# Performance work log

Measured on AMD Instinct MI355X. Metric: run time of the kernel, lower is better.

## Reference

```python
import jax, jax.numpy as jnp
import numpy as np


def setup_inputs() -> dict:
    key = jax.random.key(0)
    ks = jax.random.split(key, 20)
    B, T, E, U, D, O = 64, 2048, 256, 256, 256, 32000
    s = lambda k, shp, fan: (jax.random.normal(k, shp, jnp.float32) * (1.0 / np.sqrt(fan)))
    return {
        'inputs': jax.random.normal(ks[0], (B, D), jnp.float32),
        'stm': jax.random.normal(ks[1], (B, U), jnp.float32),
        'x_seq': jax.random.normal(ks[2], (B, T, E), jnp.float32),
        'V_a': s(ks[3], (U + E,), U + E),
        'W_a': s(ks[4], (U + E, U + E), U + E),
        'W_r': s(ks[5], (D, U), D), 'U_r': s(ks[6], (U, U), U), 'C_r': s(ks[7], (E, U), E), 'b_r': jnp.zeros((U,), jnp.float32),
        'W_z': s(ks[8], (D, U), D), 'U_z': s(ks[9], (U, U), U), 'C_z': s(ks[10], (E, U), E), 'b_z': jnp.zeros((U,), jnp.float32),
        'W_p': s(ks[11], (D, U), D), 'U_p': s(ks[12], (U, U), U), 'C_p': s(ks[13], (E, U), E), 'b_p': jnp.zeros((U,), jnp.float32),
        'W_o': s(ks[14], (D, O), D), 'U_o': s(ks[15], (U, O), U), 'C_o': s(ks[16], (E, O), E), 'b_o': jnp.zeros((O,), jnp.float32),
    }


def reference(inputs, stm, x_seq, V_a, W_a,
              W_r, U_r, C_r, b_r,
              W_z, U_z, C_z, b_z,
              W_p, U_p, C_p, b_p,
              W_o, U_o, C_o, b_o):
    B, T, E = x_seq.shape
    U = stm.shape[-1]
    # Bahdanau additive attention: concat repeated state with encoder seq
    _stm = jnp.broadcast_to(stm[:, None, :], (B, T, U))          # [B,T,U]
    cat = jnp.concatenate([_stm, x_seq], axis=-1)                 # [B,T,U+E]
    et = jnp.einsum('btc,c->bt', jnp.tanh(jnp.einsum('btc,cd->btd', cat, W_a)), V_a)
    at = jax.nn.softmax(et, axis=1)                               # exp / sum over T
    context = jnp.einsum('bt,bte->be', at, x_seq)                 # [B,E]
    # GRU-style gates conditioned on input, previous state, and context
    rt = jax.nn.sigmoid(inputs @ W_r + stm @ U_r + context @ C_r + b_r)
    zt = jax.nn.sigmoid(inputs @ W_z + stm @ U_z + context @ C_z + b_z)
    s_tp = jnp.tanh(inputs @ W_p + (rt * stm) @ U_p + context @ C_p + b_p)
    st = (1.0 - zt) * stm + zt * s_tp                             # new state [B,U]
    output = jax.nn.softmax(inputs @ W_o + stm @ U_o + context @ C_o + b_o, axis=-1)  # [B,O]
    return output, st
```

## Files before the change

### kernel.cpp

```cpp
#include <hip/hip_runtime.h>
#include <hip/hip_bf16.h>

#define B_ 64
#define T_ 2048
#define E_ 256
#define U_ 256
#define O_ 32000
#define UE_ 512

typedef __attribute__((ext_vector_type(8))) short bf16x8;
typedef __attribute__((ext_vector_type(4))) float f32x4;

__device__ __forceinline__ unsigned short f2bf(float f){
  __hip_bfloat16 h = __float2bfloat16(f);
  return __builtin_bit_cast(unsigned short, h);
}
__device__ __forceinline__ unsigned pk2bf(float a, float b){
  return (unsigned)f2bf(a) | ((unsigned)f2bf(b) << 16);
}
__device__ __forceinline__ bf16x8 pack8(const float* v0, const float* v1){
  float4 x = *(const float4*)v0;
  float4 y = *(const float4*)v1;
  uint4 pk;
  pk.x = pk2bf(x.x, x.y); pk.y = pk2bf(x.z, x.w);
  pk.z = pk2bf(y.x, y.y); pk.w = pk2bf(y.z, y.w);
  return __builtin_bit_cast(bf16x8, pk);
}
__device__ __forceinline__ float ftanh(float x){
  float e = __expf(2.0f*x);
  return 1.0f - 2.0f/(e + 1.0f);
}
__device__ __forceinline__ float fsig(float x){
  return 1.0f/(1.0f + __expf(-x));
}

__global__ __launch_bounds__(256)
void prep_kernel(const float* __restrict__ Wa, const float* __restrict__ stm,
                 unsigned short* __restrict__ bpack, float* __restrict__ sp){
  if (blockIdx.x < 64){
    int idx = blockIdx.x*256 + threadIdx.x;
    int n = idx & 511;
    int ktg = idx >> 9;
    int erow = ktg * 8;
    unsigned short o[8];
#pragma unroll
    for (int i = 0; i < 8; ++i)
      o[i] = f2bf(Wa[(256 + erow + i)*512 + n]);
    uint4 v;
    v.x = (unsigned)o[0] | ((unsigned)o[1] << 16);
    v.y = (unsigned)o[2] | ((unsigned)o[3] << 16);
    v.z = (unsigned)o[4] | ((unsigned)o[5] << 16);
    v.w = (unsigned)o[6] | ((unsigned)o[7] << 16);
    ((uint4*)bpack)[idx] = v;
  } else {
    int tid = threadIdx.x;
    int w = tid >> 6, l = tid & 63, c = l & 15, g = l >> 4;
    int n0 = (blockIdx.x - 64)*64 + w*16;
    f32x4 zero = {0.f,0.f,0.f,0.f};
    f32x4 acc[4];
#pragma unroll
    for (int mt = 0; mt < 4; ++mt) acc[mt] = zero;
#pragma unroll
    for (int ks = 0; ks < 8; ++ks){
      int kg = ks*32 + 8*g;
      bf16x8 a[4];
#pragma unroll
      for (int mt = 0; mt < 4; ++mt){
        const float* ap = stm + (mt*16 + c)*256 + kg;
        a[mt] = pack8(ap, ap + 4);
      }
      const float* bpt = Wa + (size_t)kg*512 + n0 + c;
      float bv[8];
#pragma unroll
      for (int i = 0; i < 8; ++i) bv[i] = bpt[(size_t)i*512];
      uint4 pk;
      pk.x = pk2bf(bv[0], bv[1]); pk.y = pk2bf(bv[2], bv[3]);
      pk.z = pk2bf(bv[4], bv[5]); pk.w = pk2bf(bv[6], bv[7]);
      bf16x8 bfr = __builtin_bit_cast(bf16x8, pk);
#pragma unroll
      for (int mt = 0; mt < 4; ++mt)
        acc[mt] = __builtin_amdgcn_mfma_f32_16x16x32_bf16(a[mt], bfr, acc[mt], 0, 0, 0);
    }
#pragma unroll
    for (int mt = 0; mt < 4; ++mt)
#pragma unroll
      for (int r = 0; r < 4; ++r){
        int m = mt*16 + 4*g + r;
        sp[m*512 + n0 + c] = acc[mt][r];
      }
  }
}

__global__ __launch_bounds__(512, 4)
void et_flash_kernel(const float* __restrict__ xseq, const unsigned short* __restrict__ bpack,
                     const float* __restrict__ va, const float* __restrict__ sp,
                     float* __restrict__ msbuf, float* __restrict__ uctxp){
  __shared__ __align__(16) uint4 sA4[2048];
  __shared__ float sVa[512];
  __shared__ float sSp[512];
  __shared__ float sEt[8][64];
  __shared__ float sE[64];
  int tid = threadIdx.x;
  int w = tid >> 6, l = tid & 63, c = l & 15, g = l >> 4;
  int m0 = blockIdx.x * 64;
  int b  = m0 >> 11;

  const float4* x4 = (const float4*)xseq + (size_t)m0 * 64;
  uint2* sA2 = (uint2*)sA4;
#pragma unroll
  for (int i = 0; i < 8; ++i){
    int p = i*512 + tid;
    int row = p >> 6, kq = p & 63;
    float4 v = x4[row*64 + kq];
    uint2 u;
    u.x = pk2bf(v.x, v.y);
    u.y = pk2bf(v.z, v.w);
    int s = ((row>>4)*8 + (kq>>3))*64 + ((kq>>1)&3)*16 + (row&15);
    sA2[(s ^ ((s>>4)&7))*2 + (kq&1)] = u;
  }
  sVa[tid] = va[tid];
  sSp[tid] = sp[b*512 + tid];
  __syncthreads();

  f32x4 zero = {0.f, 0.f, 0.f, 0.f};
  f32x4 acc[4][4];
#pragma unroll
  for (int mt = 0; mt < 4; ++mt)
#pragma unroll
    for (int tc = 0; tc < 4; ++tc) acc[mt][tc] = zero;

  const bf16x8* bp = (const bf16x8*)bpack;
#pragma unroll
  for (int ks = 0; ks < 8; ++ks){
    bf16x8 aw[4], bx[4];
    int bbase = (ks*4 + g)*512 + w*64 + c;
#pragma unroll
    for (int mt = 0; mt < 4; ++mt)
      aw[mt] = bp[bbase + mt*16];
#pragma unroll
    for (int tc = 0; tc < 4; ++tc){
      int idx = (tc*8 + ks)*64 + l;
      bx[tc] = *(const bf16x8*)&sA4[idx ^ ((idx>>4)&7)];
    }
#pragma unroll
    for (int mt = 0; mt < 4; ++mt)
#pragma unroll
      for (int tc = 0; tc < 4; ++tc)
        acc[mt][tc] = __builtin_amdgcn_mfma_f32_16x16x32_bf16(aw[mt], bx[tc], acc[mt][tc], 0, 0, 0);
  }

  float p[4] = {0.f, 0.f, 0.f, 0.f};
#pragma unroll
  for (int mt = 0; mt < 4; ++mt){
    int nb = w*64 + mt*16 + 4*g;
    float4 vav = *(const float4*)&sVa[nb];
    float4 spv = *(const float4*)&sSp[nb];
#pragma unroll
    for (int tc = 0; tc < 4; ++tc){
#pragma unroll
      for (int r = 0; r < 4; ++r){
        float vv = acc[mt][tc][r] + ((const float*)&spv)[r];
        p[tc] += ((const float*)&vav)[r] * ftanh(vv);
      }
    }
  }
#pragma unroll
  for (int tc = 0; tc < 4; ++tc){
    p[tc] += __shfl_xor(p[tc], 16, 64);
    p[tc] += __shfl_xor(p[tc], 32, 64);
  }
  if (l < 16){
#pragma unroll
    for (int tc = 0; tc < 4; ++tc)
      sEt[w][tc*16 + c] = p[tc];
  }
  __syncthreads();

  if (tid < 64){
    float e = 0.f;
#pragma unroll
    for (int ww = 0; ww < 8; ++ww) e += sEt[ww][tid];
    float m = e;
#pragma unroll
    for (int off = 1; off < 64; off <<= 1) m = fmaxf(m, __shfl_xor(m, off, 64));
    float ex = __expf(e - m);
    float s = ex;
#pragma unroll
    for (int off = 1; off < 64; off <<= 1) s += __shfl_xor(s, off, 64);
    sE[tid] = ex;
    if (tid == 0){
      msbuf[blockIdx.x*2]     = m;
      msbuf[blockIdx.x*2 + 1] = s;
    }
  }
  __syncthreads();

  {
    int e = tid & 255, th = tid >> 8;
    int ks = e >> 5, gg = (e >> 3) & 3, ii = e & 7;
    const unsigned short* sU = (const unsigned short*)sA4;
    float a0 = 0.f;
#pragma unroll
    for (int tt = 0; tt < 32; ++tt){
      int t = th*32 + tt;
      int mt = t >> 4, cc = t & 15;
      int slt = (mt*8 + ks)*64 + gg*16 + cc;
      unsigned short hv = sU[(size_t)(slt ^ ((slt>>4)&7))*8 + ii];
      float xv = __builtin_bit_cast(float, ((unsigned)hv) << 16);
      a0 += sE[t] * xv;
    }
    uctxp[((size_t)blockIdx.x*2 + th)*256 + e] = a0;
  }
}

__global__ void ctx_x1_kernel(const float* __restrict__ msbuf, const float* __restrict__ uctxp,
                              const float* __restrict__ inputs, const float* __restrict__ stm,
                              unsigned short* __restrict__ X1bf){
  int b = blockIdx.x, e = threadIdx.x;
  float M = -INFINITY;
#pragma unroll 4
  for (int j = 0; j < 32; ++j) M = fmaxf(M, msbuf[(32*b + j)*2]);
  float S = 0.f;
  float acc = 0.f;
#pragma unroll 4
  for (int j = 0; j < 32; ++j){
    float wj = __expf(msbuf[(32*b + j)*2] - M);
    S += msbuf[(32*b + j)*2 + 1] * wj;
    size_t base = ((size_t)(32*b + j)*2)*256 + e;
    acc += (uctxp[base] + uctxp[base + 256]) * wj;
  }
  float ctx = acc / S;
  X1bf[b*768 + e]        = f2bf(inputs[b*256 + e]);
  X1bf[b*768 + 256 + e]  = f2bf(stm[b*256 + e]);
  X1bf[b*768 + 512 + e]  = f2bf(ctx);
}

__global__ __launch_bounds__(256)
void gates1_kernel(const unsigned short* __restrict__ X1bf, const float* __restrict__ stm,
                   const float* __restrict__ Wr, const float* __restrict__ Ur,
                   const float* __restrict__ Cr, const float* __restrict__ brr,
                   const float* __restrict__ Wz, const float* __restrict__ Uz,
                   const float* __restrict__ Cz, const float* __restrict__ bzz,
                   const float* __restrict__ Wp, const float* __restrict__ Cp,
                   const float* __restrict__ bpp,
                   float* __restrict__ rs, float* __restrict__ ztb, float* __restrict__ pic){
  int tid = threadIdx.x;
  int w = tid >> 6, l = tid & 63, c = l & 15, g = l >> 4;
  int n0 = blockIdx.x*64 + w*16;
  int gate = n0 >> 8;
  int col0 = n0 & 255;
  const float* W0; const float* W1; const float* W2; const float* bias;
  if (gate == 0){ W0 = Wr; W1 = Ur; W2 = Cr; bias = brr; }
  else if (gate == 1){ W0 = Wz; W1 = Uz; W2 = Cz; bias = bzz; }
  else { W0 = Wp; W1 = nullptr; W2 = Cp; bias = bpp; }

  f32x4 zero = {0.f,0.f,0.f,0.f};
  f32x4 acc[4];
#pragma unroll
  for (int mt = 0; mt < 4; ++mt) acc[mt] = zero;

#pragma unroll
  for (int ph = 0; ph < 3; ++ph){
    const float* src = (ph == 0) ? W0 : (ph == 1) ? W1 : W2;
    if (src == nullptr) continue;
#pragma unroll
    for (int ks = 0; ks < 8; ++ks){
      int kg = ks*32 + 8*g;
      bf16x8 a[4];
#pragma unroll
      for (int mt = 0; mt < 4; ++mt)
        a[mt] = *(const bf16x8*)&X1bf[(mt*16 + c)*768 + ph*256 + kg];
      const float* bpt = src + (size_t)kg*256 + col0 + c;
      float bv[8];
#pragma unroll
      for (int i = 0; i < 8; ++i) bv[i] = bpt[(size_t)i*256];
      uint4 pk;
      pk.x = pk2bf(bv[0], bv[1]); pk.y = pk2bf(bv[2], bv[3]);
      pk.z = pk2bf(bv[4], bv[5]); pk.w = pk2bf(bv[6], bv[7]);
      bf16x8 bfr = __builtin_bit_cast(bf16x8, pk);
#pragma unroll
      for (int mt = 0; mt < 4; ++mt)
        acc[mt] = __builtin_amdgcn_mfma_f32_16x16x32_bf16(a[mt], bfr, acc[mt], 0, 0, 0);
    }
  }

  int n = col0 + c;
  float bi = bias[n];
#pragma unroll
  for (int mt = 0; mt < 4; ++mt)
#pragma unroll
    for (int r = 0; r < 4; ++r){
      int m = mt*16 + 4*g + r;
      float pre = acc[mt][r] + bi;
      if (gate == 0)      rs[m*256 + n]  = fsig(pre) * stm[m*256 + n];
      else if (gate == 1) ztb[m*256 + n] = fsig(pre);
      else                pic[m*256 + n] = pre;
    }
}

__global__ __launch_bounds__(256)
void gates2_kernel(const float* __restrict__ rs, const float* __restrict__ Up,
                   const float* __restrict__ pic, const float* __restrict__ ztb,
                   const float* __restrict__ stm, float* __restrict__ stout){
  int tid = threadIdx.x;
  int w = tid >> 6, l = tid & 63, c = l & 15, g = l >> 4;
  int n0 = blockIdx.x*64 + w*16;
  f32x4 zero = {0.f,0.f,0.f,0.f};
  f32x4 acc[4];
#pragma unroll
  for (int mt = 0; mt < 4; ++mt) acc[mt] = zero;
#pragma unroll
  for (int ks = 0; ks < 8; ++ks){
    int kg = ks*32 + 8*g;
    bf16x8 a[4];
#pragma unroll
    for (int mt = 0; mt < 4; ++mt){
      const float* ap = rs + (mt*16 + c)*256 + kg;
      a[mt] = pack8(ap, ap + 4);
    }
    const float* bpt = Up + (size_t)kg*256 + n0 + c;
    float bv[8];
#pragma unroll
    for (int i = 0; i < 8; ++i) bv[i] = bpt[(size_t)i*256];
    uint4 pk;
    pk.x = pk2bf(bv[0], bv[1]); pk.y = pk2bf(bv[2], bv[3]);
    pk.z = pk2bf(bv[4], bv[5]); pk.w = pk2bf(bv[6], bv[7]);
    bf16x8 bfr = __builtin_bit_cast(bf16x8, pk);
#pragma unroll
    for (int mt = 0; mt < 4; ++mt)
      acc[mt] = __builtin_amdgcn_mfma_f32_16x16x32_bf16(a[mt], bfr, acc[mt], 0, 0, 0);
  }
#pragma unroll
  for (int mt = 0; mt < 4; ++mt)
#pragma unroll
    for (int r = 0; r < 4; ++r){
      int m = mt*16 + 4*g + r;
      int o = m*256 + n0 + c;
      float ap = pic[o] + acc[mt][r];
      float z = ztb[o];
      stout[o] = (1.f - z)*stm[o] + z*ftanh(ap);
    }
}

__global__ __launch_bounds__(512)
void logits_mfma_kernel(const unsigned short* __restrict__ X1bf,
                        const float* __restrict__ Wo, const float* __restrict__ Uo,
                        const float* __restrict__ Co, const float* __restrict__ boo,
                        float* __restrict__ outl){
  __shared__ float sAcc[16][4][64];
  int tid = threadIdx.x;
  int w = tid >> 6, l = tid & 63, c = l & 15, g = l >> 4;
  int wc = w & 3;
  int kh = w >> 2;
  int n0 = blockIdx.x*64 + wc*16;
  f32x4 zero = {0.f,0.f,0.f,0.f};
  f32x4 acc[4];
#pragma unroll
  for (int mt = 0; mt < 4; ++mt) acc[mt] = zero;

#pragma unroll
  for (int ph = 0; ph < 3; ++ph){
    const float* src = (ph == 0) ? Wo : (ph == 1) ? Uo : Co;
#pragma unroll
    for (int kss = 0; kss < 4; ++kss){
      int ks = 2*kss + kh;
      int kg = ph*256 + ks*32 + 8*g;
      bf16x8 a[4];
#pragma unroll
      for (int mt = 0; mt < 4; ++mt)
        a[mt] = *(const bf16x8*)&X1bf[(mt*16 + c)*768 + kg];
      const float* bpt = src + (size_t)(ks*32 + 8*g)*32000 + n0 + c;
      float bv[8];
#pragma unroll
      for (int i = 0; i < 8; ++i) bv[i] = bpt[(size_t)i*32000];
      uint4 pk;
      pk.x = pk2bf(bv[0], bv[1]);
      pk.y = pk2bf(bv[2], bv[3]);
      pk.z = pk2bf(bv[4], bv[5]);
      pk.w = pk2bf(bv[6], bv[7]);
      bf16x8 bfr = __builtin_bit_cast(bf16x8, pk);
#pragma unroll
      for (int mt = 0; mt < 4; ++mt)
        acc[mt] = __builtin_amdgcn_mfma_f32_16x16x32_bf16(a[mt], bfr, acc[mt], 0, 0, 0);
    }
  }

  if (kh == 1){
#pragma unroll
    for (int mt = 0; mt < 4; ++mt)
#pragma unroll
      for (int r = 0; r < 4; ++r)
        sAcc[mt*4 + r][wc][l] = acc[mt][r];
  }
  __syncthreads();
  if (kh == 0){
    float bias = boo[n0 + c];
#pragma unroll
    for (int mt = 0; mt < 4; ++mt)
#pragma unroll
      for (int r = 0; r < 4; ++r){
        int m = mt*16 + 4*g + r;
        float vv = acc[mt][r] + sAcc[mt*4 + r][wc][l] + bias;
        outl[(size_t)m*32000 + n0 + c] = vv;
      }
  }
}

__global__ void sm_part_kernel(const float* __restrict__ logits, float* __restrict__ part){
  __shared__ float red[4];
  __shared__ float red2[4];
  int bid = blockIdx.x;
  int b = bid >> 3, ch = bid & 7;
  int base = b*32000 + ch*4000;
  int tid = threadIdx.x;
  float v[16];
#pragma unroll
  for (int i = 0; i < 16; ++i){
    int idx = i*256 + tid;
    v[i] = (idx < 4000) ? logits[base + idx] : -INFINITY;
  }
  float m = v[0];
#pragma unroll
  for (int i = 1; i < 16; ++i) m = fmaxf(m, v[i]);
#pragma unroll
  for (int off = 1; off < 64; off <<= 1) m = fmaxf(m, __shfl_xor(m, off, 64));
  int wv = tid >> 6;
  if ((tid & 63) == 0) red[wv] = m;
  __syncthreads();
  m = fmaxf(fmaxf(red[0], red[1]), fmaxf(red[2], red[3]));
  float s = 0.f;
#pragma unroll
  for (int i = 0; i < 16; ++i) s += __expf(v[i] - m);
#pragma unroll
  for (int off = 1; off < 64; off <<= 1) s += __shfl_xor(s, off, 64);
  if ((tid & 63) == 0) red2[wv] = s;
  __syncthreads();
  if (tid == 0){
    float st = red2[0] + red2[1] + red2[2] + red2[3];
    part[bid*2]     = m;
    part[bid*2 + 1] = st;
  }
}

__global__ void sm_norm_kernel(float* __restrict__ logits, const float* __restrict__ part){
  int bid = blockIdx.x;
  int b = bid >> 3, ch = bid & 7;
  int base = b*32000 + ch*4000;
  int tid = threadIdx.x;
  float M = -INFINITY;
#pragma unroll
  for (int cc = 0; cc < 8; ++cc) M = fmaxf(M, part[(b*8 + cc)*2]);
  float S = 0.f;
#pragma unroll
  for (int cc = 0; cc < 8; ++cc) S += part[(b*8 + cc)*2 + 1] * __expf(part[(b*8 + cc)*2] - M);
  float inv = 1.0f / S;
#pragma unroll
  for (int i = 0; i < 16; ++i){
    int idx = i*256 + tid;
    if (idx < 4000){
      int o = base + idx;
      logits[o] = __expf(logits[o] - M) * inv;
    }
  }
}

extern "C" void kernel_launch(void* const* d_in, const int* in_sizes, int n_in,
                              void* d_out, int out_size, void* d_ws, size_t ws_size,
                              hipStream_t stream) {
  const float* inputs = (const float*)d_in[0];
  const float* stm    = (const float*)d_in[1];
  const float* xseq   = (const float*)d_in[2];
  const float* Va     = (const float*)d_in[3];
  const float* Wa     = (const float*)d_in[4];
  const float* Wr = (const float*)d_in[5];
  const float* Ur = (const float*)d_in[6];
  const float* Cr = (const float*)d_in[7];
  const float* br = (const float*)d_in[8];
  const float* Wz = (const float*)d_in[9];
  const float* Uz = (const float*)d_in[10];
  const float* Cz = (const float*)d_in[11];
  const float* bz = (const float*)d_in[12];
  const float* Wp = (const float*)d_in[13];
  const float* Up = (const float*)d_in[14];
  const float* Cp = (const float*)d_in[15];
  const float* bp = (const float*)d_in[16];
  const float* Wo = (const float*)d_in[17];
  const float* Uo = (const float*)d_in[18];
  const float* Co = (const float*)d_in[19];
  const float* bo = (const float*)d_in[20];

  float* out   = (float*)d_out;
  float* stout = out + (size_t)B_*O_;

  float* wsf = (float*)d_ws;
  unsigned short* bpack = (unsigned short*)d_ws;
  float* sp    = wsf + 65536;
  float* msbuf = wsf + 98304;
  float* uctxp = wsf + 102400;
  unsigned short* X1bf = (unsigned short*)(wsf + 1150976);
  float* part  = wsf + 1175552;
  float* rs    = wsf + 1176576;
  float* ztb   = wsf + 1192960;
  float* pic   = wsf + 1209344;

  prep_kernel<<<72, 256, 0, stream>>>(Wa, stm, bpack, sp);
  et_flash_kernel<<<2048, 512, 0, stream>>>(xseq, bpack, Va, sp, msbuf, uctxp);
  ctx_x1_kernel<<<64, 256, 0, stream>>>(msbuf, uctxp, inputs, stm, X1bf);
  gates1_kernel<<<12, 256, 0, stream>>>(X1bf, stm, Wr, Ur, Cr, br,
                                        Wz, Uz, Cz, bz, Wp, Cp, bp,
                                        rs, ztb, pic);
  gates2_kernel<<<4, 256, 0, stream>>>(rs, Up, pic, ztb, stm, stout);
  logits_mfma_kernel<<<500, 512, 0, stream>>>(X1bf, Wo, Uo, Co, bo, out);
  sm_part_kernel<<<512, 256, 0, stream>>>(out, part);
  sm_norm_kernel<<<512, 256, 0, stream>>>(out, part);
}
```

Baseline: 163.7 us.

## Fuse softmax partial max/sum into logits kernel and raise MFMA priority

The logits GEMM kernel now computes per-block row max and exp-sum partials while the values are still in registers. This removes the separate sm_part pass that re-read the full 64x32000 logits array, and a small combine kernel merges the 500 partials per row. It also wraps the MFMA loop in the attention kernel with s_setprio to favor matrix issue. The cost is extra shuffles and syncs in the logits epilogue, plus a reuse of the msbuf/uctxp workspace regions for the partial buffers.

```diff
diff --git a/kernel.cpp b/kernel.cpp
--- a/kernel.cpp
+++ b/kernel.cpp
@@ -142,11 +142,13 @@
       int idx = (tc*8 + ks)*64 + l;
       bx[tc] = *(const bf16x8*)&sA4[idx ^ ((idx>>4)&7)];
     }
+    __builtin_amdgcn_s_setprio(1);
 #pragma unroll
     for (int mt = 0; mt < 4; ++mt)
 #pragma unroll
       for (int tc = 0; tc < 4; ++tc)
         acc[mt][tc] = __builtin_amdgcn_mfma_f32_16x16x32_bf16(aw[mt], bx[tc], acc[mt][tc], 0, 0, 0);
+    __builtin_amdgcn_s_setprio(0);
   }
 
   float p[4] = {0.f, 0.f, 0.f, 0.f};
@@ -346,8 +348,10 @@
 void logits_mfma_kernel(const unsigned short* __restrict__ X1bf,
                         const float* __restrict__ Wo, const float* __restrict__ Uo,
                         const float* __restrict__ Co, const float* __restrict__ boo,
-                        float* __restrict__ outl){
+                        float* __restrict__ outl, float* __restrict__ part2){
   __shared__ float sAcc[16][4][64];
+  __shared__ float sMx[4][64];
+  __shared__ float sSx[4][64];
   int tid = threadIdx.x;
   int w = tid >> 6, l = tid & 63, c = l & 15, g = l >> 4;
   int wc = w & 3;
@@ -393,67 +397,113 @@
         sAcc[mt*4 + r][wc][l] = acc[mt][r];
   }
   __syncthreads();
-  if (kh == 0){
+
+  bool active = (kh == 0);
+  float vv[4][4];
+  if (active){
     float bias = boo[n0 + c];
 #pragma unroll
     for (int mt = 0; mt < 4; ++mt)
 #pragma unroll
       for (int r = 0; r < 4; ++r){
         int m = mt*16 + 4*g + r;
-        float vv = acc[mt][r] + sAcc[mt*4 + r][wc][l] + bias;
-        outl[(size_t)m*32000 + n0 + c] = vv;
+        vv[mt][r] = acc[mt][r] + sAcc[mt*4 + r][wc][l] + bias;
+        outl[(size_t)m*32000 + n0 + c] = vv[mt][r];
       }
-  }
-}
-
-__global__ void sm_part_kernel(const float* __restrict__ logits, float* __restrict__ part){
-  __shared__ float red[4];
-  __shared__ float red2[4];
+    float mx[4][4];
+#pragma unroll
+    for (int mt = 0; mt < 4; ++mt)
+#pragma unroll
+      for (int r = 0; r < 4; ++r) mx[mt][r] = vv[mt][r];
+#pragma unroll
+    for (int mask = 1; mask < 16; mask <<= 1)
+#pragma unroll
+      for (int mt = 0; mt < 4; ++mt)
+#pragma unroll
+        for (int r = 0; r < 4; ++r)
+          mx[mt][r] = fmaxf(mx[mt][r], __shfl_xor(mx[mt][r], mask, 64));
+    if (c == 0)
+#pragma unroll
+      for (int mt = 0; mt < 4; ++mt)
+#pragma unroll
+        for (int r = 0; r < 4; ++r)
+          sMx[wc][mt*16 + 4*g + r] = mx[mt][r];
+  }
+  __syncthreads();
+  if (active){
+    float sx[4][4];
+#pragma unroll
+    for (int mt = 0; mt < 4; ++mt)
+#pragma unroll
+      for (int r = 0; r < 4; ++r){
+        int row = mt*16 + 4*g + r;
+        float M = fmaxf(fmaxf(sMx[0][row], sMx[1][row]), fmaxf(sMx[2][row], sMx[3][row]));
+        sx[mt][r] = __expf(vv[mt][r] - M);
+      }
+#pragma unroll
+    for (int mask = 1; mask < 16; mask <<= 1)
+#pragma unroll
+      for (int mt = 0; mt < 4; ++mt)
+#pragma unroll
+        for (int r = 0; r < 4; ++r)
+          sx[mt][r] += __shfl_xor(sx[mt][r], mask, 64);
+    if (c == 0)
+#pragma unroll
+      for (int mt = 0; mt < 4; ++mt)
+#pragma unroll
+        for (int r = 0; r < 4; ++r)
+          sSx[wc][mt*16 + 4*g + r] = sx[mt][r];
+  }
+  __syncthreads();
+  if (tid < 64){
+    int row = tid;
+    float M = fmaxf(fmaxf(sMx[0][row], sMx[1][row]), fmaxf(sMx[2][row], sMx[3][row]));
+    float S = sSx[0][row] + sSx[1][row] + sSx[2][row] + sSx[3][row];
+    part2[((size_t)blockIdx.x*64 + row)*2]     = M;
+    part2[((size_t)blockIdx.x*64 + row)*2 + 1] = S;
+  }
+}
+
+__global__ void sm_comb_kernel(const float* __restrict__ part2, float* __restrict__ fin){
+  __shared__ float red[8];
+  __shared__ float red2[8];
+  int b = blockIdx.x;
+  int tid = threadIdx.x;
+  float M = -INFINITY, S = 0.f;
+  if (tid < 500){
+    M = part2[((size_t)tid*64 + b)*2];
+    S = part2[((size_t)tid*64 + b)*2 + 1];
+  }
+  float m1 = M;
+#pragma unroll
+  for (int off = 1; off < 64; off <<= 1) m1 = fmaxf(m1, __shfl_xor(m1, off, 64));
+  int wv = tid >> 6;
+  if ((tid & 63) == 0) red[wv] = m1;
+  __syncthreads();
+  float Mg = red[0];
+#pragma unroll
+  for (int i = 1; i < 8; ++i) Mg = fmaxf(Mg, red[i]);
+  float s1 = (tid < 500) ? S * __expf(M - Mg) : 0.f;
+#pragma unroll
+  for (int off = 1; off < 64; off <<= 1) s1 += __shfl_xor(s1, off, 64);
+  if ((tid & 63) == 0) red2[wv] = s1;
+  __syncthreads();
+  if (tid == 0){
+    float St = 0.f;
+#pragma unroll
+    for (int i = 0; i < 8; ++i) St += red2[i];
+    fin[b*2] = Mg;
+    fin[b*2 + 1] = St;
+  }
+}
+
+__global__ void sm_norm_kernel(float* __restrict__ logits, const float* __restrict__ fin){
   int bid = blockIdx.x;
   int b = bid >> 3, ch = bid & 7;
   int base = b*32000 + ch*4000;
   int tid = threadIdx.x;
-  float v[16];
-#pragma unroll
-  for (int i = 0; i < 16; ++i){
-    int idx = i*256 + tid;
-    v[i] = (idx < 4000) ? logits[base + idx] : -INFINITY;
-  }
-  float m = v[0];
-#pragma unroll
-  for (int i = 1; i < 16; ++i) m = fmaxf(m, v[i]);
-#pragma unroll
-  for (int off = 1; off < 64; off <<= 1) m = fmaxf(m, __shfl_xor(m, off, 64));
-  int wv = tid >> 6;
-  if ((tid & 63) == 0) red[wv] = m;
-  __syncthreads();
-  m = fmaxf(fmaxf(red[0], red[1]), fmaxf(red[2], red[3]));
-  float s = 0.f;
-#pragma unroll
-  for (int i = 0; i < 16; ++i) s += __expf(v[i] - m);
-#pragma unroll
-  for (int off = 1; off < 64; off <<= 1) s += __shfl_xor(s, off, 64);
-  if ((tid & 63) == 0) red2[wv] = s;
-  __syncthreads();
-  if (tid == 0){
-    float st = red2[0] + red2[1] + red2[2] + red2[3];
-    part[bid*2]     = m;
-    part[bid*2 + 1] = st;
-  }
-}
-
-__global__ void sm_norm_kernel(float* __restrict__ logits, const float* __restrict__ part){
-  int bid = blockIdx.x;
-  int b = bid >> 3, ch = bid & 7;
-  int base = b*32000 + ch*4000;
-  int tid = threadIdx.x;
-  float M = -INFINITY;
-#pragma unroll
-  for (int cc = 0; cc < 8; ++cc) M = fmaxf(M, part[(b*8 + cc)*2]);
-  float S = 0.f;
-#pragma unroll
-  for (int cc = 0; cc < 8; ++cc) S += part[(b*8 + cc)*2 + 1] * __expf(part[(b*8 + cc)*2] - M);
-  float inv = 1.0f / S;
+  float M = fin[2*b];
+  float inv = 1.0f / fin[2*b + 1];
 #pragma unroll
   for (int i = 0; i < 16; ++i){
     int idx = i*256 + tid;
@@ -497,8 +547,9 @@
   float* sp    = wsf + 65536;
   float* msbuf = wsf + 98304;
   float* uctxp = wsf + 102400;
+  float* fin   = wsf + 98304;
+  float* part2 = wsf + 102400;
   unsigned short* X1bf = (unsigned short*)(wsf + 1150976);
-  float* part  = wsf + 1175552;
   float* rs    = wsf + 1176576;
   float* ztb   = wsf + 1192960;
   float* pic   = wsf + 1209344;
@@ -510,7 +561,7 @@
                                         Wz, Uz, Cz, bz, Wp, Cp, bp,
                                         rs, ztb, pic);
   gates2_kernel<<<4, 256, 0, stream>>>(rs, Up, pic, ztb, stm, stout);
-  logits_mfma_kernel<<<500, 512, 0, stream>>>(X1bf, Wo, Uo, Co, bo, out);
-  sm_part_kernel<<<512, 256, 0, stream>>>(out, part);
-  sm_norm_kernel<<<512, 256, 0, stream>>>(out, part);
-}
+  logits_mfma_kernel<<<500, 512, 0, stream>>>(X1bf, Wo, Uo, Co, bo, out, part2);
+  sm_comb_kernel<<<64, 512, 0, stream>>>(part2, fin);
+  sm_norm_kernel<<<512, 256, 0, stream>>>(out, fin);
+}
```

New measurement: 162.3 us. Within noise of the previous version (-0.9%).
